# Kernel tuning notes

Measured on AMD Instinct MI355X. Metric: run time of the kernel, lower is better.

## Reference

```python
import jax, jax.numpy as jnp
import numpy as np

N_NODES = 100000
D_IN = 64
D_OUT = 64
N_EDGES = 1250000


def setup_inputs() -> dict:
    key = jax.random.key(0)
    k_x, k_e, k_wl, k_bl, k_wr = jax.random.split(key, 5)
    x = jax.random.normal(k_x, (N_NODES, D_IN), dtype=jnp.float32)
    edge_index = jax.random.randint(k_e, (2, N_EDGES), 0, N_NODES, dtype=jnp.int64)
    # SAGEConv params: lin_l (neighbor transform, with bias), lin_r (root transform, no bias)
    s_in = 1.0 / np.sqrt(D_IN)
    W_l = jax.random.uniform(k_wl, (D_IN, D_OUT), dtype=jnp.float32, minval=-s_in, maxval=s_in)
    b_l = jax.random.uniform(k_bl, (D_OUT,), dtype=jnp.float32, minval=-s_in, maxval=s_in)
    W_r = jax.random.uniform(k_wr, (D_IN, D_OUT), dtype=jnp.float32, minval=-s_in, maxval=s_in)
    return {"x": x, "edge_index": edge_index, "W_l": W_l, "b_l": b_l, "W_r": W_r}


def reference(x, edge_index, W_l, b_l, W_r):
    # PyG SAGEConv with aggr='add':
    #   out = lin_l(sum_{j in N(i)} x_j) + lin_r(x_i), then tanh
    src = edge_index[0]  # message sources (x_j)
    dst = edge_index[1]  # message targets (i)
    msg = x[src]                                             # [E, D_IN] gather
    aggr = jax.ops.segment_sum(msg, dst, num_segments=x.shape[0])  # [N, D_IN] scatter-add
    out = aggr @ W_l + b_l + x @ W_r                         # [N, D_OUT]
    return jnp.tanh(out)
```

## Files before the change

### kernel.cpp

```cpp
#include <hip/hip_runtime.h>
#include <hip/hip_bf16.h>
#include <hip/hip_fp16.h>

#define N_NODES 100000
#define D 64
#define N_EDGES 1250000

#define RB 64
#define NB 1563
#define FCAP 1536
#define SORT_CAP 1536

#define CB_SHIFT 11
#define NCB 49
#define CCAP 28672
#define FINE_PER_COARSE 32

#define EPB 8192
#define PARTA_BLOCKS ((N_EDGES + EPB - 1) / EPB)
#define SEGS 8

typedef unsigned short ushort_t;

__device__ __forceinline__ ushort_t f2h(float f) {
    return __half_as_ushort(__float2half_rn(f));
}

#define TN 64
#define FS 68

__global__ __launch_bounds__(256) void pre_kernel(
    const float* __restrict__ x, const float* __restrict__ W_l,
    const float* __restrict__ b_l, const float* __restrict__ W_r,
    ushort_t* __restrict__ y, float* __restrict__ zout,
    int* __restrict__ ccursor, int* __restrict__ fcursor, int N)
{
    __shared__ float sW[2 * 64 * 64];
    __shared__ float sX[TN * FS];

    int t = threadIdx.x;
    if (blockIdx.x == 0) {
        for (int i = t; i < NCB; i += 256) ccursor[i] = 0;
        for (int i = t; i < NB; i += 256) fcursor[i] = 0;
    }
    for (int i = t; i < 64 * 64; i += 256) {
        sW[i] = W_l[i];
        sW[4096 + i] = W_r[i];
    }

    long base = (long)blockIdx.x * TN;
    for (int i = t; i < TN * 16; i += 256) {
        int n = i >> 4, q = i & 15;
        long node = base + n;
        float4 v = make_float4(0.f, 0.f, 0.f, 0.f);
        if (node < N) v = ((const float4*)(x + node * D))[q];
        *(float4*)&sX[n * FS + q * 4] = v;
    }
    __syncthreads();

    const int og = (t & 15) * 4;
    const int ng = (t >> 4) * 4;
    float4 b = *(const float4*)(b_l + og);

    float accL[4][4], accR[4][4];
#pragma unroll
    for (int i = 0; i < 4; i++) {
        accL[i][0] = 0.f; accL[i][1] = 0.f; accL[i][2] = 0.f; accL[i][3] = 0.f;
        accR[i][0] = b.x; accR[i][1] = b.y; accR[i][2] = b.z; accR[i][3] = b.w;
    }

#pragma unroll 2
    for (int k = 0; k < 64; k += 4) {
        float4 wl[4], wr[4], a[4];
#pragma unroll
        for (int j = 0; j < 4; j++) {
            wl[j] = *(const float4*)&sW[(k + j) * 64 + og];
            wr[j] = *(const float4*)&sW[4096 + (k + j) * 64 + og];
        }
#pragma unroll
        for (int i = 0; i < 4; i++) a[i] = *(const float4*)&sX[(ng + i) * FS + k];
#pragma unroll
        for (int i = 0; i < 4; i++) {
            float av[4] = {a[i].x, a[i].y, a[i].z, a[i].w};
#pragma unroll
            for (int j = 0; j < 4; j++) {
                accL[i][0] += av[j] * wl[j].x;
                accL[i][1] += av[j] * wl[j].y;
                accL[i][2] += av[j] * wl[j].z;
                accL[i][3] += av[j] * wl[j].w;
                accR[i][0] += av[j] * wr[j].x;
                accR[i][1] += av[j] * wr[j].y;
                accR[i][2] += av[j] * wr[j].z;
                accR[i][3] += av[j] * wr[j].w;
            }
        }
    }

#pragma unroll
    for (int i = 0; i < 4; i++) {
        long node = base + ng + i;
        if (node < N) {
            ushort4 py;
            py.x = f2h(accL[i][0]); py.y = f2h(accL[i][1]);
            py.z = f2h(accL[i][2]); py.w = f2h(accL[i][3]);
            *(ushort4*)(y + node * D + og) = py;
            float4 pz = make_float4(accR[i][0], accR[i][1], accR[i][2], accR[i][3]);
            *(float4*)(zout + node * D + og) = pz;
        }
    }
}

__global__ __launch_bounds__(256) void partA_kernel(
    const int* __restrict__ src, const int* __restrict__ dst,
    int* __restrict__ ccursor, unsigned* __restrict__ coarse, int E)
{
    __shared__ int hist[NCB];
    __shared__ int bbase[NCB];
    int t = threadIdx.x;
    if (t < NCB) hist[t] = 0;
    __syncthreads();

    int base = blockIdx.x * EPB;
    int lim = E - base; if (lim > EPB) lim = EPB;

    for (int i = t; i < lim; i += 256) {
        int d = dst[base + i];
        atomicAdd(&hist[d >> CB_SHIFT], 1);
    }
    __syncthreads();

    if (t < NCB) {
        int c = hist[t];
        bbase[t] = c ? atomicAdd(&ccursor[t], c) : 0;
    }
    __syncthreads();

    for (int i = t; i < lim; i += 256) {
        int d = dst[base + i];
        int s = src[base + i];
        int b = d >> CB_SHIFT;
        int pos = atomicSub(&hist[b], 1) - 1;
        coarse[(size_t)b * CCAP + bbase[b] + pos] =
            (unsigned)s | ((unsigned)(d & ((1 << CB_SHIFT) - 1)) << 17);
    }
}

__global__ __launch_bounds__(256) void partB_kernel(
    const unsigned* __restrict__ coarse, const int* __restrict__ ccursor,
    int* __restrict__ fcursor, unsigned* __restrict__ fine)
{
    __shared__ int hist[FINE_PER_COARSE];
    __shared__ int bbase[FINE_PER_COARSE];
    int cb = blockIdx.x >> 3;
    int seg = blockIdx.x & 7;
    int t = threadIdx.x;

    int cnt = ccursor[cb];
    int segLen = (cnt + SEGS - 1) / SEGS;
    int beg = seg * segLen;
    int end = beg + segLen; if (end > cnt) end = cnt;

    if (t < FINE_PER_COARSE) hist[t] = 0;
    __syncthreads();

    const unsigned* __restrict__ slab = coarse + (size_t)cb * CCAP;

    for (int i = beg + t; i < end; i += 256) {
        unsigned e = slab[i];
        atomicAdd(&hist[(e >> 17) >> 6], 1);
    }
    __syncthreads();

    if (t < FINE_PER_COARSE) {
        int c = hist[t];
        int fb = cb * FINE_PER_COARSE + t;
        bbase[t] = c ? atomicAdd(&fcursor[fb], c) : 0;
    }
    __syncthreads();

    for (int i = beg + t; i < end; i += 256) {
        unsigned e = slab[i];
        unsigned cl = e >> 17;
        int fb_loc = cl >> 6;
        int pos = atomicSub(&hist[fb_loc], 1) - 1;
        size_t fb = (size_t)cb * FINE_PER_COARSE + fb_loc;
        fine[fb * FCAP + bbase[fb_loc] + pos] =
            (e & 0x1FFFFu) | ((cl & 63u) << 17);
    }
}

__global__ __launch_bounds__(512) void sortgather_kernel(
    const ushort_t* __restrict__ y, const unsigned* __restrict__ part,
    const int* __restrict__ cursor, float* __restrict__ out, int N)
{
    __shared__ int sorted[SORT_CAP];
    __shared__ int hist[RB];
    __shared__ int scanv[RB];
    __shared__ int cur[RB];
    __shared__ int begL[RB];

    int b = blockIdx.x;
    int t = threadIdx.x;
    int cnt = cursor[b];
    if (cnt > SORT_CAP) cnt = SORT_CAP;
    const unsigned* __restrict__ slab = part + (size_t)b * FCAP;

    unsigned e0 = 0, e1 = 0, e2 = 0;
    int i0 = t, i1 = t + 512, i2 = t + 1024;
    if (i0 < cnt) e0 = slab[i0];
    if (i1 < cnt) e1 = slab[i1];
    if (i2 < cnt) e2 = slab[i2];

    if (t < RB) hist[t] = 0;
    __syncthreads();

    if (i0 < cnt) atomicAdd(&hist[e0 >> 17], 1);
    if (i1 < cnt) atomicAdd(&hist[e1 >> 17], 1);
    if (i2 < cnt) atomicAdd(&hist[e2 >> 17], 1);
    __syncthreads();

    if (t < RB) scanv[t] = hist[t];
    __syncthreads();
#pragma unroll
    for (int off = 1; off < RB; off <<= 1) {
        int v = 0;
        if (t < RB && t >= off) v = scanv[t - off];
        __syncthreads();
        if (t < RB) scanv[t] += v;
        __syncthreads();
    }
    if (t < RB) {
        int ex = scanv[t] - hist[t];
        cur[t] = ex;
        begL[t] = ex;
    }
    __syncthreads();

    if (i0 < cnt) { int p = atomicAdd(&cur[e0 >> 17], 1); sorted[p] = (int)(e0 & 0x1FFFF); }
    if (i1 < cnt) { int p = atomicAdd(&cur[e1 >> 17], 1); sorted[p] = (int)(e1 & 0x1FFFF); }
    if (i2 < cnt) { int p = atomicAdd(&cur[e2 >> 17], 1); sorted[p] = (int)(e2 & 0x1FFFF); }
    __syncthreads();

    const int g = t >> 3;
    const int f = t & 7;
    int myBeg = begL[g];
    int myDeg = hist[g];

    float2 acc0 = make_float2(0.f, 0.f), acc1 = acc0, acc2 = acc0, acc3 = acc0;

    int i = 0;
    for (; i + 4 <= myDeg; i += 4) {
        int s0 = sorted[myBeg + i];
        int s1 = sorted[myBeg + i + 1];
        int s2 = sorted[myBeg + i + 2];
        int s3 = sorted[myBeg + i + 3];
        uint4 r0 = ((const uint4*)(y + (size_t)s0 * D))[f];
        uint4 r1 = ((const uint4*)(y + (size_t)s1 * D))[f];
        uint4 r2 = ((const uint4*)(y + (size_t)s2 * D))[f];
        uint4 r3 = ((const uint4*)(y + (size_t)s3 * D))[f];
#define ACC(r) { \
        float2 c0 = __half22float2(*(const __half2*)&(r).x); \
        float2 c1 = __half22float2(*(const __half2*)&(r).y); \
        float2 c2 = __half22float2(*(const __half2*)&(r).z); \
        float2 c3 = __half22float2(*(const __half2*)&(r).w); \
        acc0.x += c0.x; acc0.y += c0.y; acc1.x += c1.x; acc1.y += c1.y; \
        acc2.x += c2.x; acc2.y += c2.y; acc3.x += c3.x; acc3.y += c3.y; }
        ACC(r0) ACC(r1) ACC(r2) ACC(r3)
    }
    for (; i < myDeg; i++) {
        int s = sorted[myBeg + i];
        uint4 r = ((const uint4*)(y + (size_t)s * D))[f];
        ACC(r)
    }
#undef ACC

    long gn = (long)b * RB + g;
    if (gn < N) {
        float4* op = (float4*)(out + gn * D);
        float4 z0 = op[2 * f];
        float4 z1 = op[2 * f + 1];
        float4 o0, o1;
        o0.x = tanhf(acc0.x + z0.x); o0.y = tanhf(acc0.y + z0.y);
        o0.z = tanhf(acc1.x + z0.z); o0.w = tanhf(acc1.y + z0.w);
        o1.x = tanhf(acc2.x + z1.x); o1.y = tanhf(acc2.y + z1.y);
        o1.z = tanhf(acc3.x + z1.z); o1.w = tanhf(acc3.y + z1.w);
        op[2 * f] = o0;
        op[2 * f + 1] = o1;
    }
}

extern "C" void kernel_launch(void* const* d_in, const int* in_sizes, int n_in,
                              void* d_out, int out_size, void* d_ws, size_t ws_size,
                              hipStream_t stream) {
    const float* x   = (const float*)d_in[0];
    const int* ei    = (const int*)d_in[1];
    const float* W_l = (const float*)d_in[2];
    const float* b_l = (const float*)d_in[3];
    const float* W_r = (const float*)d_in[4];
    float* out = (float*)d_out;

    const int N = N_NODES;
    const int E = N_EDGES;
    const int* src = ei;
    const int* dst = ei + E;

    char* ws = (char*)d_ws;
    ushort_t* y      = (ushort_t*)(ws);
    unsigned* coarse = (unsigned*)(ws + 12800000);
    unsigned* fine   = (unsigned*)(ws + 18419712);
    int* ccursor     = (int*)(ws + 28022784);
    int* fcursor     = (int*)(ws + 28023040);

    pre_kernel<<<(N + TN - 1) / TN, 256, 0, stream>>>(
        x, W_l, b_l, W_r, y, out, ccursor, fcursor, N);
    partA_kernel<<<PARTA_BLOCKS, 256, 0, stream>>>(src, dst, ccursor, coarse, E);
    partB_kernel<<<NCB * SEGS, 256, 0, stream>>>(coarse, ccursor, fcursor, fine);
    sortgather_kernel<<<NB, 512, 0, stream>>>(y, fine, fcursor, out, N);
}
```

Measured before the change: 172.3 us.

## Fuse dense transform with coarse edge partition and store root term in fp16

Merges the dense precompute kernel and the coarse edge-partitioning kernel into one launch, with block index selecting the role, so the two independent stages overlap on the GPU. Cursor zeroing moves to a memset, since the fused kernel no longer runs before the partition. The root transform output is stored as fp16 in a separate workspace buffer instead of fp32 in the output, which halves that write and read traffic. The cost is extra fp16 rounding error on the root term, and the fused kernel's occupancy is set by the larger shared memory of the dense path.

```diff
diff --git a/kernel.cpp b/kernel.cpp
--- a/kernel.cpp
+++ b/kernel.cpp
@@ -20,6 +20,9 @@
 #define PARTA_BLOCKS ((N_EDGES + EPB - 1) / EPB)
 #define SEGS 8
 
+#define PRE_BLOCKS 1563
+#define FUSED_BLOCKS (PARTA_BLOCKS + PRE_BLOCKS)
+
 typedef unsigned short ushort_t;
 
 __device__ __forceinline__ ushort_t f2h(float f) {
@@ -29,26 +32,57 @@
 #define TN 64
 #define FS 68
 
-__global__ __launch_bounds__(256) void pre_kernel(
+__global__ __launch_bounds__(256) void pre_part_kernel(
     const float* __restrict__ x, const float* __restrict__ W_l,
     const float* __restrict__ b_l, const float* __restrict__ W_r,
-    ushort_t* __restrict__ y, float* __restrict__ zout,
-    int* __restrict__ ccursor, int* __restrict__ fcursor, int N)
+    ushort_t* __restrict__ y, ushort_t* __restrict__ z,
+    const int* __restrict__ src, const int* __restrict__ dst,
+    int* __restrict__ ccursor, unsigned* __restrict__ coarse,
+    int N, int E)
 {
+    int t = threadIdx.x;
+
+    if (blockIdx.x < PARTA_BLOCKS) {
+        __shared__ int hist[NCB];
+        __shared__ int bbase[NCB];
+        if (t < NCB) hist[t] = 0;
+        __syncthreads();
+
+        int base = blockIdx.x * EPB;
+        int lim = E - base; if (lim > EPB) lim = EPB;
+
+        for (int i = t; i < lim; i += 256) {
+            int d = dst[base + i];
+            atomicAdd(&hist[d >> CB_SHIFT], 1);
+        }
+        __syncthreads();
+
+        if (t < NCB) {
+            int c = hist[t];
+            bbase[t] = c ? atomicAdd(&ccursor[t], c) : 0;
+        }
+        __syncthreads();
+
+        for (int i = t; i < lim; i += 256) {
+            int d = dst[base + i];
+            int s = src[base + i];
+            int b = d >> CB_SHIFT;
+            int pos = atomicSub(&hist[b], 1) - 1;
+            coarse[(size_t)b * CCAP + bbase[b] + pos] =
+                (unsigned)s | ((unsigned)(d & ((1 << CB_SHIFT) - 1)) << 17);
+        }
+        return;
+    }
+
     __shared__ float sW[2 * 64 * 64];
     __shared__ float sX[TN * FS];
 
-    int t = threadIdx.x;
-    if (blockIdx.x == 0) {
-        for (int i = t; i < NCB; i += 256) ccursor[i] = 0;
-        for (int i = t; i < NB; i += 256) fcursor[i] = 0;
-    }
     for (int i = t; i < 64 * 64; i += 256) {
         sW[i] = W_l[i];
         sW[4096 + i] = W_r[i];
     }
 
-    long base = (long)blockIdx.x * TN;
+    long base = (long)(blockIdx.x - PARTA_BLOCKS) * TN;
     for (int i = t; i < TN * 16; i += 256) {
         int n = i >> 4, q = i & 15;
         long node = base + n;
@@ -100,48 +134,14 @@
     for (int i = 0; i < 4; i++) {
         long node = base + ng + i;
         if (node < N) {
-            ushort4 py;
+            ushort4 py, pz;
             py.x = f2h(accL[i][0]); py.y = f2h(accL[i][1]);
             py.z = f2h(accL[i][2]); py.w = f2h(accL[i][3]);
+            pz.x = f2h(accR[i][0]); pz.y = f2h(accR[i][1]);
+            pz.z = f2h(accR[i][2]); pz.w = f2h(accR[i][3]);
             *(ushort4*)(y + node * D + og) = py;
-            float4 pz = make_float4(accR[i][0], accR[i][1], accR[i][2], accR[i][3]);
-            *(float4*)(zout + node * D + og) = pz;
-        }
-    }
-}
-
-__global__ __launch_bounds__(256) void partA_kernel(
-    const int* __restrict__ src, const int* __restrict__ dst,
-    int* __restrict__ ccursor, unsigned* __restrict__ coarse, int E)
-{
-    __shared__ int hist[NCB];
-    __shared__ int bbase[NCB];
-    int t = threadIdx.x;
-    if (t < NCB) hist[t] = 0;
-    __syncthreads();
-
-    int base = blockIdx.x * EPB;
-    int lim = E - base; if (lim > EPB) lim = EPB;
-
-    for (int i = t; i < lim; i += 256) {
-        int d = dst[base + i];
-        atomicAdd(&hist[d >> CB_SHIFT], 1);
-    }
-    __syncthreads();
-
-    if (t < NCB) {
-        int c = hist[t];
-        bbase[t] = c ? atomicAdd(&ccursor[t], c) : 0;
-    }
-    __syncthreads();
-
-    for (int i = t; i < lim; i += 256) {
-        int d = dst[base + i];
-        int s = src[base + i];
-        int b = d >> CB_SHIFT;
-        int pos = atomicSub(&hist[b], 1) - 1;
-        coarse[(size_t)b * CCAP + bbase[b] + pos] =
-            (unsigned)s | ((unsigned)(d & ((1 << CB_SHIFT) - 1)) << 17);
+            *(ushort4*)(z + node * D + og) = pz;
+        }
     }
 }
 
@@ -190,8 +190,9 @@
 }
 
 __global__ __launch_bounds__(512) void sortgather_kernel(
-    const ushort_t* __restrict__ y, const unsigned* __restrict__ part,
-    const int* __restrict__ cursor, float* __restrict__ out, int N)
+    const ushort_t* __restrict__ y, const ushort_t* __restrict__ z,
+    const unsigned* __restrict__ part, const int* __restrict__ cursor,
+    float* __restrict__ out, int N)
 {
     __shared__ int sorted[SORT_CAP];
     __shared__ int hist[RB];
@@ -276,14 +277,17 @@
 
     long gn = (long)b * RB + g;
     if (gn < N) {
-        float4* op = (float4*)(out + gn * D);
-        float4 z0 = op[2 * f];
-        float4 z1 = op[2 * f + 1];
+        uint4 zr = ((const uint4*)(z + (size_t)gn * D))[f];
+        float2 z0 = __half22float2(*(const __half2*)&zr.x);
+        float2 z1 = __half22float2(*(const __half2*)&zr.y);
+        float2 z2 = __half22float2(*(const __half2*)&zr.z);
+        float2 z3 = __half22float2(*(const __half2*)&zr.w);
         float4 o0, o1;
         o0.x = tanhf(acc0.x + z0.x); o0.y = tanhf(acc0.y + z0.y);
-        o0.z = tanhf(acc1.x + z0.z); o0.w = tanhf(acc1.y + z0.w);
-        o1.x = tanhf(acc2.x + z1.x); o1.y = tanhf(acc2.y + z1.y);
-        o1.z = tanhf(acc3.x + z1.z); o1.w = tanhf(acc3.y + z1.w);
+        o0.z = tanhf(acc1.x + z1.x); o0.w = tanhf(acc1.y + z1.y);
+        o1.x = tanhf(acc2.x + z2.x); o1.y = tanhf(acc2.y + z2.y);
+        o1.z = tanhf(acc3.x + z3.x); o1.w = tanhf(acc3.y + z3.y);
+        float4* op = (float4*)(out + gn * D);
         op[2 * f] = o0;
         op[2 * f + 1] = o1;
     }
@@ -306,14 +310,16 @@
 
     char* ws = (char*)d_ws;
     ushort_t* y      = (ushort_t*)(ws);
-    unsigned* coarse = (unsigned*)(ws + 12800000);
-    unsigned* fine   = (unsigned*)(ws + 18419712);
-    int* ccursor     = (int*)(ws + 28022784);
-    int* fcursor     = (int*)(ws + 28023040);
-
-    pre_kernel<<<(N + TN - 1) / TN, 256, 0, stream>>>(
-        x, W_l, b_l, W_r, y, out, ccursor, fcursor, N);
-    partA_kernel<<<PARTA_BLOCKS, 256, 0, stream>>>(src, dst, ccursor, coarse, E);
+    ushort_t* z      = (ushort_t*)(ws + 12800000);
+    unsigned* coarse = (unsigned*)(ws + 25600000);
+    unsigned* fine   = (unsigned*)(ws + 31219712);
+    int* ccursor     = (int*)(ws + 40822784);
+    int* fcursor     = (int*)(ws + 40823040);
+
+    hipMemsetAsync(ccursor, 0, 6508, stream);
+
+    pre_part_kernel<<<FUSED_BLOCKS, 256, 0, stream>>>(
+        x, W_l, b_l, W_r, y, z, src, dst, ccursor, coarse, N, E);
     partB_kernel<<<NCB * SEGS, 256, 0, stream>>>(coarse, ccursor, fcursor, fine);
-    sortgather_kernel<<<NB, 512, 0, stream>>>(y, fine, fcursor, out, N);
-}
+    sortgather_kernel<<<NB, 512, 0, stream>>>(y, z, fine, fcursor, out, N);
+}
```

Measured after the change: 151.1 us. 1.14x faster.
